# Kernel tuning notes

Hardware: AMD Instinct MI355X
Metric: run time of the kernel (lower is better)

## Reference

```python
import jax, jax.numpy as jnp
import numpy as np

B, T, I, H, L, C = 256, 512, 128, 256, 2, 1000


def _uniform(key, shape, k):
    return jax.random.uniform(key, shape, jnp.float32, -k, k)


def setup_inputs() -> dict:
    key = jax.random.key(0)
    ks = jax.random.split(key, 12)
    k = 1.0 / np.sqrt(H)
    return {
        "x": jax.random.normal(ks[0], (B, T, I), jnp.float32),
        # layer 0 (PyTorch LSTM param layout: W_ih [4H, in], W_hh [4H, H], biases [4H])
        "Wih0": _uniform(ks[1], (4 * H, I), k),
        "Whh0": _uniform(ks[2], (4 * H, H), k),
        "bih0": _uniform(ks[3], (4 * H,), k),
        "bhh0": _uniform(ks[4], (4 * H,), k),
        # layer 1
        "Wih1": _uniform(ks[5], (4 * H, H), k),
        "Whh1": _uniform(ks[6], (4 * H, H), k),
        "bih1": _uniform(ks[7], (4 * H,), k),
        "bhh1": _uniform(ks[8], (4 * H,), k),
        # final classifier
        "fcW": _uniform(ks[9], (C, H), k),
        "fcb": _uniform(ks[10], (C,), k),
    }


def _lstm_layer(seq, Wih, Whh, bias):
    # seq: [B, T, in]; returns hidden sequence [B, T, H]
    b, t = seq.shape[0], seq.shape[1]
    h_dim = Whh.shape[1]
    # Precompute input projection for all timesteps (one big GEMM).
    x_proj = jnp.einsum('bti,gi->btg', seq, Wih) + bias  # [B, T, 4H]

    def step(carry, xp):
        h, c = carry
        gates = xp + h @ Whh.T                     # [B, 4H]
        i, f, g, o = jnp.split(gates, 4, axis=-1)  # PyTorch gate order i,f,g,o
        i = jax.nn.sigmoid(i)
        f = jax.nn.sigmoid(f)
        g = jnp.tanh(g)
        o = jax.nn.sigmoid(o)
        c = f * c + i * g
        h = o * jnp.tanh(c)
        return (h, c), h

    h0 = jnp.zeros((b, h_dim), seq.dtype)
    c0 = jnp.zeros((b, h_dim), seq.dtype)
    _, hs = jax.lax.scan(step, (h0, c0), jnp.swapaxes(x_proj, 0, 1))  # [T, B, H]
    return jnp.swapaxes(hs, 0, 1)


def reference(x, Wih0, Whh0, bih0, bhh0, Wih1, Whh1, bih1, bhh1, fcW, fcb):
    out = _lstm_layer(x, Wih0, Whh0, bih0 + bhh0)
    out = _lstm_layer(out, Wih1, Whh1, bih1 + bhh1)
    # classifier on last timestep
    return out[:, -1, :] @ fcW.T + fcb  # [B, C]
```

## Files before the change

kernel.cpp:

```cpp
#include <hip/hip_runtime.h>

#define B_ 256
#define T_ 512
#define I_ 128
#define H_ 256
#define C_ 1000

#define RSTR 17

#define WT_OFF   393216
#define WT_FLOATS 917504
#define WS_NEED_FLOATS (WT_OFF + WT_FLOATS)

__device__ __forceinline__ float fsig(float x) { return 1.0f / (1.0f + __expf(-x)); }
__device__ __forceinline__ float ftanh(float x) { return 2.0f / (1.0f + __expf(-2.0f * x)) - 1.0f; }

__global__ __launch_bounds__(256) void transpose_w(
    const float* __restrict__ Wih0, const float* __restrict__ Whh0,
    const float* __restrict__ Wih1, const float* __restrict__ Whh1,
    float* __restrict__ ws)
{
    int idx = blockIdx.x * 256 + threadIdx.x;
    float* wt = ws + WT_OFF;
    if (idx < 131072) { int k = idx >> 10, r = idx & 1023; wt[idx] = Wih0[r * I_ + k]; return; }
    idx -= 131072; wt += 131072;
    if (idx < 262144) { int k = idx >> 10, r = idx & 1023; wt[idx] = Whh0[r * H_ + k]; return; }
    idx -= 262144; wt += 262144;
    if (idx < 262144) { int k = idx >> 10, r = idx & 1023; wt[idx] = Wih1[r * H_ + k]; return; }
    idx -= 262144; wt += 262144;
    { int k = idx >> 10, r = idx & 1023; wt[idx] = Whh1[r * H_ + k]; }
}

__global__ __launch_bounds__(256) void lstm_step_t(
    const float* __restrict__ x,
    const float* __restrict__ bih0, const float* __restrict__ bhh0,
    const float* __restrict__ bih1, const float* __restrict__ bhh1,
    float* __restrict__ ws, int s)
{
    __shared__ float As[128 * 36];
    __shared__ float Wsh[128 * 36];

    float* h0t = ws;
    float* h1t = ws + 2 * B_ * H_;
    float* c0 = ws + 4 * B_ * H_;
    float* c1 = ws + 5 * B_ * H_;

    const int w = blockIdx.x;
    const int layer = w >> 8;
    const int r = w & 255;
    const int bb = r >> 5;
    const int hb = r & 31;

    if (layer == 0 && s >= T_) return;
    if (layer == 1 && s < 1) return;
    const int t = (layer == 0) ? s : (s - 1);

    const float* hprev_t; const float* h0cur_t = nullptr;
    float* hout_t; float* cbuf;
    const float* bi; const float* bh;
    const float* wt_ih; const float* wt_hh;
    int nchunks;
    if (layer == 0) {
        hprev_t = h0t + ((t - 1) & 1) * B_ * H_;
        hout_t  = h0t + (t & 1) * B_ * H_;
        cbuf = c0; bi = bih0; bh = bhh0;
        wt_ih = ws + WT_OFF;
        wt_hh = ws + WT_OFF + 131072;
        nchunks = 3;
    } else {
        h0cur_t = h0t + (t & 1) * B_ * H_;
        hprev_t = h1t + ((t - 1) & 1) * B_ * H_;
        hout_t  = h1t + (t & 1) * B_ * H_;
        cbuf = c1; bi = bih1; bh = bhh1;
        wt_ih = ws + WT_OFF + 393216;
        wt_hh = ws + WT_OFF + 655360;
        nchunks = 4;
    }

    const int tid = threadIdx.x;
    const int srow = tid >> 3;
    const int kv = tid & 7;
    const int wave = tid >> 6;
    const int lane = tid & 63;
    const int br = lane >> 3;
    const int gc8 = lane & 7;
    const int krow = tid >> 1;
    const int half = tid & 1;

    float acc[4][4];
#pragma unroll
    for (int a = 0; a < 4; ++a)
#pragma unroll
        for (int b = 0; b < 4; ++b) acc[a][b] = 0.0f;

    for (int cc = 0; cc < nchunks; ++cc) {
        if (layer == 0 && cc == 0) {
            const float* ap = x + ((size_t)(bb * 32 + srow) * T_ + t) * I_;
#pragma unroll
            for (int i = 0; i < 4; ++i) {
                const int k4 = (kv + 8 * i) * 4;
                float4 va = *(const float4*)(ap + k4);
                As[(k4 + 0) * 36 + srow] = va.x;
                As[(k4 + 1) * 36 + srow] = va.y;
                As[(k4 + 2) * 36 + srow] = va.z;
                As[(k4 + 3) * 36 + srow] = va.w;
            }
        } else {
            const float* hsrc; int k0;
            if (layer == 0) { hsrc = hprev_t; k0 = (cc - 1) * 128; }
            else if (cc < 2) { hsrc = h0cur_t; k0 = cc * 128; }
            else             { hsrc = hprev_t; k0 = (cc - 2) * 128; }
            const float* asrc = hsrc + (size_t)(k0 + krow) * B_ + bb * 32 + half * 16;
            float4 a0 = ((const float4*)asrc)[0];
            float4 a1 = ((const float4*)asrc)[1];
            float4 a2 = ((const float4*)asrc)[2];
            float4 a3 = ((const float4*)asrc)[3];
            float* adst = As + krow * 36 + half * 16;
            ((float4*)adst)[0] = a0;
            ((float4*)adst)[1] = a1;
            ((float4*)adst)[2] = a2;
            ((float4*)adst)[3] = a3;
        }
        {
            const float* wtc; int k0w;
            if (layer == 0) {
                if (cc == 0) { wtc = wt_ih; k0w = 0; }
                else         { wtc = wt_hh; k0w = (cc - 1) * 128; }
            } else {
                if (cc < 2)  { wtc = wt_ih; k0w = cc * 128; }
                else         { wtc = wt_hh; k0w = (cc - 2) * 128; }
            }
            const float* wsrc = wtc + (size_t)(k0w + krow) * 1024 + (2 * half) * 256 + hb * 8;
            float4 w0 = ((const float4*)wsrc)[0];
            float4 w1 = ((const float4*)wsrc)[1];
            float4 w2 = ((const float4*)(wsrc + 256))[0];
            float4 w3 = ((const float4*)(wsrc + 256))[1];
            float* wdst = Wsh + krow * 36 + half * 16;
            ((float4*)wdst)[0] = w0;
            ((float4*)wdst)[1] = w1;
            ((float4*)wdst)[2] = w2;
            ((float4*)wdst)[3] = w3;
        }
        __syncthreads();
        const float* Ap = &As[(wave * 32) * 36 + br * 4];
        const float* Wp = &Wsh[(wave * 32) * 36 + gc8 * 4];
#pragma unroll
        for (int kk = 0; kk < 32; ++kk) {
            float4 a = *(const float4*)(Ap + kk * 36);
            float4 wv = *(const float4*)(Wp + kk * 36);
            acc[0][0] += a.x * wv.x; acc[0][1] += a.x * wv.y; acc[0][2] += a.x * wv.z; acc[0][3] += a.x * wv.w;
            acc[1][0] += a.y * wv.x; acc[1][1] += a.y * wv.y; acc[1][2] += a.y * wv.z; acc[1][3] += a.y * wv.w;
            acc[2][0] += a.z * wv.x; acc[2][1] += a.z * wv.y; acc[2][2] += a.z * wv.z; acc[2][3] += a.z * wv.w;
            acc[3][0] += a.w * wv.x; acc[3][1] += a.w * wv.y; acc[3][2] += a.w * wv.z; acc[3][3] += a.w * wv.w;
        }
        __syncthreads();
    }

    float* red = As;
    {
        const int base = tid * RSTR;
#pragma unroll
        for (int a = 0; a < 4; ++a)
#pragma unroll
            for (int b = 0; b < 4; ++b)
                red[base + a * 4 + b] = acc[a][b];
    }
    __syncthreads();
    {
        const int bl = tid >> 3;
        const int j = tid & 7;
        float g4[4];
#pragma unroll
        for (int g = 0; g < 4; ++g) {
            const int gc = g * 8 + j;
            const int br2 = bl >> 2, bi2 = bl & 3, gq = gc >> 2, gj = gc & 3;
            float v = 0.0f;
#pragma unroll
            for (int wv = 0; wv < 4; ++wv)
                v += red[(wv * 64 + br2 * 8 + gq) * RSTR + bi2 * 4 + gj];
            const int growg = g * H_ + hb * 8 + j;
            v += bi[growg] + bh[growg];
            g4[g] = v;
        }
        const float ig = fsig(g4[0]);
        const float fg = fsig(g4[1]);
        const float gg = ftanh(g4[2]);
        const float og = fsig(g4[3]);
        const int b = bb * 32 + bl;
        const int hidx = hb * 8 + j;
        const int ci = b * H_ + hidx;
        const float cn = fg * cbuf[ci] + ig * gg;
        cbuf[ci] = cn;
        hout_t[(size_t)hidx * B_ + b] = og * ftanh(cn);
    }
}

__global__ __launch_bounds__(256) void fc_kernel_t(
    const float* __restrict__ ws, const float* __restrict__ fcW,
    const float* __restrict__ fcb, float* __restrict__ out)
{
    __shared__ float As[128 * 36];
    __shared__ float Wsh[128 * 36];

    const float* h1 = ws + 3 * B_ * H_;
    const int bb = blockIdx.x >> 5;
    const int cb = blockIdx.x & 31;
    const int tid = threadIdx.x;
    const int srow = tid >> 3;
    const int kv = tid & 7;
    const int wave = tid >> 6;
    const int lane = tid & 63;
    const int br = lane >> 3;
    const int gc8 = lane & 7;
    const int crow = cb * 32 + srow;
    const int krow = tid >> 1;
    const int half = tid & 1;

    float acc[4][4];
#pragma unroll
    for (int a = 0; a < 4; ++a)
#pragma unroll
        for (int b = 0; b < 4; ++b) acc[a][b] = 0.0f;

    for (int cc = 0; cc < 2; ++cc) {
        {
            const float* asrc = h1 + (size_t)(cc * 128 + krow) * B_ + bb * 32 + half * 16;
            float4 a0 = ((const float4*)asrc)[0];
            float4 a1 = ((const float4*)asrc)[1];
            float4 a2 = ((const float4*)asrc)[2];
            float4 a3 = ((const float4*)asrc)[3];
            float* adst = As + krow * 36 + half * 16;
            ((float4*)adst)[0] = a0;
            ((float4*)adst)[1] = a1;
            ((float4*)adst)[2] = a2;
            ((float4*)adst)[3] = a3;
        }
#pragma unroll
        for (int i = 0; i < 4; ++i) {
            const int k4 = (kv + 8 * i) * 4;
            float4 vw = make_float4(0.f, 0.f, 0.f, 0.f);
            if (crow < C_) vw = *(const float4*)(fcW + crow * H_ + cc * 128 + k4);
            Wsh[(k4 + 0) * 36 + srow] = vw.x;
            Wsh[(k4 + 1) * 36 + srow] = vw.y;
            Wsh[(k4 + 2) * 36 + srow] = vw.z;
            Wsh[(k4 + 3) * 36 + srow] = vw.w;
        }
        __syncthreads();
        const float* Ap = &As[(wave * 32) * 36 + br * 4];
        const float* Wp = &Wsh[(wave * 32) * 36 + gc8 * 4];
#pragma unroll
        for (int kk = 0; kk < 32; ++kk) {
            float4 a = *(const float4*)(Ap + kk * 36);
            float4 wv = *(const float4*)(Wp + kk * 36);
            acc[0][0] += a.x * wv.x; acc[0][1] += a.x * wv.y; acc[0][2] += a.x * wv.z; acc[0][3] += a.x * wv.w;
            acc[1][0] += a.y * wv.x; acc[1][1] += a.y * wv.y; acc[1][2] += a.y * wv.z; acc[1][3] += a.y * wv.w;
            acc[2][0] += a.z * wv.x; acc[2][1] += a.z * wv.y; acc[2][2] += a.z * wv.z; acc[2][3] += a.z * wv.w;
            acc[3][0] += a.w * wv.x; acc[3][1] += a.w * wv.y; acc[3][2] += a.w * wv.z; acc[3][3] += a.w * wv.w;
        }
        __syncthreads();
    }

    float* red = As;
    {
        const int base = tid * RSTR;
#pragma unroll
        for (int a = 0; a < 4; ++a)
#pragma unroll
            for (int b = 0; b < 4; ++b)
                red[base + a * 4 + b] = acc[a][b];
    }
    __syncthreads();
    {
        const int bl = tid >> 3;
        const int j = tid & 7;
#pragma unroll
        for (int g = 0; g < 4; ++g) {
            const int gc = g * 8 + j;
            const int br2 = bl >> 2, bi2 = bl & 3, gq = gc >> 2, gj = gc & 3;
            float v = 0.0f;
#pragma unroll
            for (int wv = 0; wv < 4; ++wv)
                v += red[(wv * 64 + br2 * 8 + gq) * RSTR + bi2 * 4 + gj];
            const int cglob = cb * 32 + gc;
            if (cglob < C_) {
                v += fcb[cglob];
                out[(size_t)(bb * 32 + bl) * C_ + cglob] = v;
            }
        }
    }
}

__global__ __launch_bounds__(256) void lstm_step(
    const float* __restrict__ x,
    const float* __restrict__ Wih0, const float* __restrict__ Whh0,
    const float* __restrict__ bih0, const float* __restrict__ bhh0,
    const float* __restrict__ Wih1, const float* __restrict__ Whh1,
    const float* __restrict__ bih1, const float* __restrict__ bhh1,
    float* __restrict__ ws, int s)
{
    __shared__ float As[128 * 36];
    __shared__ float Wsh[128 * 36];

    float* h0buf = ws;
    float* h1buf = ws + 2 * B_ * H_;
    float* c0 = ws + 4 * B_ * H_;
    float* c1 = ws + 5 * B_ * H_;

    const int w = blockIdx.x;
    const int layer = w >> 8;
    const int r = w & 255;
    const int bb = r >> 5;
    const int hb = r & 31;

    if (layer == 0 && s >= T_) return;
    if (layer == 1 && s < 1) return;
    const int t = (layer == 0) ? s : (s - 1);

    const float* hprev; const float* h0cur = nullptr;
    float* hout; float* cbuf;
    const float* Wih; const float* Whh; const float* bi; const float* bh;
    int nchunks;
    if (layer == 0) {
        hprev = h0buf + ((t - 1) & 1) * B_ * H_;
        hout  = h0buf + (t & 1) * B_ * H_;
        cbuf = c0; Wih = Wih0; Whh = Whh0; bi = bih0; bh = bhh0;
        nchunks = 3;
    } else {
        h0cur = h0buf + (t & 1) * B_ * H_;
        hprev = h1buf + ((t - 1) & 1) * B_ * H_;
        hout  = h1buf + (t & 1) * B_ * H_;
        cbuf = c1; Wih = Wih1; Whh = Whh1; bi = bih1; bh = bhh1;
        nchunks = 4;
    }

    const int tid = threadIdx.x;
    const int srow = tid >> 3;
    const int kv = tid & 7;
    const int wave = tid >> 6;
    const int lane = tid & 63;
    const int br = lane >> 3;
    const int gc8 = lane & 7;
    const int grow = (srow >> 3) * H_ + hb * 8 + (srow & 7);

    float acc[4][4];
#pragma unroll
    for (int a = 0; a < 4; ++a)
#pragma unroll
        for (int b = 0; b < 4; ++b) acc[a][b] = 0.0f;

    for (int cc = 0; cc < nchunks; ++cc) {
        const float* ap;
        const float* wp;
        if (layer == 0) {
            if (cc == 0) { ap = x + ((size_t)(bb * 32 + srow) * T_ + t) * I_; wp = Wih + grow * I_; }
            else         { ap = hprev + (bb * 32 + srow) * H_ + (cc - 1) * 128; wp = Whh + grow * H_ + (cc - 1) * 128; }
        } else {
            if (cc < 2)  { ap = h0cur + (bb * 32 + srow) * H_ + cc * 128;       wp = Wih + grow * H_ + cc * 128; }
            else         { ap = hprev + (bb * 32 + srow) * H_ + (cc - 2) * 128; wp = Whh + grow * H_ + (cc - 2) * 128; }
        }
#pragma unroll
        for (int i = 0; i < 4; ++i) {
            const int k4 = (kv + 8 * i) * 4;
            float4 va = *(const float4*)(ap + k4);
            As[(k4 + 0) * 36 + srow] = va.x;
            As[(k4 + 1) * 36 + srow] = va.y;
            As[(k4 + 2) * 36 + srow] = va.z;
            As[(k4 + 3) * 36 + srow] = va.w;
            float4 vw = *(const float4*)(wp + k4);
            Wsh[(k4 + 0) * 36 + srow] = vw.x;
            Wsh[(k4 + 1) * 36 + srow] = vw.y;
            Wsh[(k4 + 2) * 36 + srow] = vw.z;
            Wsh[(k4 + 3) * 36 + srow] = vw.w;
        }
        __syncthreads();
        const float* Ap = &As[(wave * 32) * 36 + br * 4];
        const float* Wp = &Wsh[(wave * 32) * 36 + gc8 * 4];
#pragma unroll
        for (int kk = 0; kk < 32; ++kk) {
            float4 a = *(const float4*)(Ap + kk * 36);
            float4 wv = *(const float4*)(Wp + kk * 36);
            acc[0][0] += a.x * wv.x; acc[0][1] += a.x * wv.y; acc[0][2] += a.x * wv.z; acc[0][3] += a.x * wv.w;
            acc[1][0] += a.y * wv.x; acc[1][1] += a.y * wv.y; acc[1][2] += a.y * wv.z; acc[1][3] += a.y * wv.w;
            acc[2][0] += a.z * wv.x; acc[2][1] += a.z * wv.y; acc[2][2] += a.z * wv.z; acc[2][3] += a.z * wv.w;
            acc[3][0] += a.w * wv.x; acc[3][1] += a.w * wv.y; acc[3][2] += a.w * wv.z; acc[3][3] += a.w * wv.w;
        }
        __syncthreads();
    }

    float* red = As;
    {
        const int base = tid * RSTR;
#pragma unroll
        for (int a = 0; a < 4; ++a)
#pragma unroll
            for (int b = 0; b < 4; ++b)
                red[base + a * 4 + b] = acc[a][b];
    }
    __syncthreads();
    {
        const int bl = tid >> 3;
        const int j = tid & 7;
        float g4[4];
#pragma unroll
        for (int g = 0; g < 4; ++g) {
            const int gc = g * 8 + j;
            const int br2 = bl >> 2, bi2 = bl & 3, gq = gc >> 2, gj = gc & 3;
            float v = 0.0f;
#pragma unroll
            for (int wv = 0; wv < 4; ++wv)
                v += red[(wv * 64 + br2 * 8 + gq) * RSTR + bi2 * 4 + gj];
            const int growg = g * H_ + hb * 8 + j;
            v += bi[growg] + bh[growg];
            g4[g] = v;
        }
        const float ig = fsig(g4[0]);
        const float fg = fsig(g4[1]);
        const float gg = ftanh(g4[2]);
        const float og = fsig(g4[3]);
        const int b = bb * 32 + bl;
        const int hidx = hb * 8 + j;
        const int ci = b * H_ + hidx;
        const float cn = fg * cbuf[ci] + ig * gg;
        cbuf[ci] = cn;
        hout[ci] = og * ftanh(cn);
    }
}

__global__ __launch_bounds__(256) void fc_kernel(
    const float* __restrict__ ws, const float* __restrict__ fcW,
    const float* __restrict__ fcb, float* __restrict__ out)
{
    __shared__ float As[128 * 36];
    __shared__ float Wsh[128 * 36];

    const float* h1 = ws + 3 * B_ * H_;
    const int bb = blockIdx.x >> 5;
    const int cb = blockIdx.x & 31;
    const int tid = threadIdx.x;
    const int srow = tid >> 3;
    const int kv = tid & 7;
    const int wave = tid >> 6;
    const int lane = tid & 63;
    const int br = lane >> 3;
    const int gc8 = lane & 7;
    const int crow = cb * 32 + srow;

    float acc[4][4];
#pragma unroll
    for (int a = 0; a < 4; ++a)
#pragma unroll
        for (int b = 0; b < 4; ++b) acc[a][b] = 0.0f;

    for (int cc = 0; cc < 2; ++cc) {
        const float* ap = h1 + (bb * 32 + srow) * H_ + cc * 128;
#pragma unroll
        for (int i = 0; i < 4; ++i) {
            const int k4 = (kv + 8 * i) * 4;
            float4 va = *(const float4*)(ap + k4);
            As[(k4 + 0) * 36 + srow] = va.x;
            As[(k4 + 1) * 36 + srow] = va.y;
            As[(k4 + 2) * 36 + srow] = va.z;
            As[(k4 + 3) * 36 + srow] = va.w;
            float4 vw = make_float4(0.f, 0.f, 0.f, 0.f);
            if (crow < C_) vw = *(const float4*)(fcW + crow * H_ + cc * 128 + k4);
            Wsh[(k4 + 0) * 36 + srow] = vw.x;
            Wsh[(k4 + 1) * 36 + srow] = vw.y;
            Wsh[(k4 + 2) * 36 + srow] = vw.z;
            Wsh[(k4 + 3) * 36 + srow] = vw.w;
        }
        __syncthreads();
        const float* Ap = &As[(wave * 32) * 36 + br * 4];
        const float* Wp = &Wsh[(wave * 32) * 36 + gc8 * 4];
#pragma unroll
        for (int kk = 0; kk < 32; ++kk) {
            float4 a = *(const float4*)(Ap + kk * 36);
            float4 wv = *(const float4*)(Wp + kk * 36);
            acc[0][0] += a.x * wv.x; acc[0][1] += a.x * wv.y; acc[0][2] += a.x * wv.z; acc[0][3] += a.x * wv.w;
            acc[1][0] += a.y * wv.x; acc[1][1] += a.y * wv.y; acc[1][2] += a.y * wv.z; acc[1][3] += a.y * wv.w;
            acc[2][0] += a.z * wv.x; acc[2][1] += a.z * wv.y; acc[2][2] += a.z * wv.z; acc[2][3] += a.z * wv.w;
            acc[3][0] += a.w * wv.x; acc[3][1] += a.w * wv.y; acc[3][2] += a.w * wv.z; acc[3][3] += a.w * wv.w;
        }
        __syncthreads();
    }

    float* red = As;
    {
        const int base = tid * RSTR;
#pragma unroll
        for (int a = 0; a < 4; ++a)
#pragma unroll
            for (int b = 0; b < 4; ++b)
                red[base + a * 4 + b] = acc[a][b];
    }
    __syncthreads();
    {
        const int bl = tid >> 3;
        const int j = tid & 7;
#pragma unroll
        for (int g = 0; g < 4; ++g) {
            const int gc = g * 8 + j;
            const int br2 = bl >> 2, bi2 = bl & 3, gq = gc >> 2, gj = gc & 3;
            float v = 0.0f;
#pragma unroll
            for (int wv = 0; wv < 4; ++wv)
                v += red[(wv * 64 + br2 * 8 + gq) * RSTR + bi2 * 4 + gj];
            const int cglob = cb * 32 + gc;
            if (cglob < C_) {
                v += fcb[cglob];
                out[(size_t)(bb * 32 + bl) * C_ + cglob] = v;
            }
        }
    }
}

extern "C" void kernel_launch(void* const* d_in, const int* in_sizes, int n_in,
                              void* d_out, int out_size, void* d_ws, size_t ws_size,
                              hipStream_t stream)
{
    const float* x    = (const float*)d_in[0];
    const float* Wih0 = (const float*)d_in[1];
    const float* Whh0 = (const float*)d_in[2];
    const float* bih0 = (const float*)d_in[3];
    const float* bhh0 = (const float*)d_in[4];
    const float* Wih1 = (const float*)d_in[5];
    const float* Whh1 = (const float*)d_in[6];
    const float* bih1 = (const float*)d_in[7];
    const float* bhh1 = (const float*)d_in[8];
    const float* fcW  = (const float*)d_in[9];
    const float* fcb  = (const float*)d_in[10];
    float* ws  = (float*)d_ws;
    float* out = (float*)d_out;

    hipMemsetAsync(d_ws, 0, (size_t)6 * B_ * H_ * sizeof(float), stream);

    const bool use_t = ws_size >= (size_t)WS_NEED_FLOATS * sizeof(float);

    if (use_t) {
        transpose_w<<<WT_FLOATS / 256, 256, 0, stream>>>(Wih0, Whh0, Wih1, Whh1, ws);
        for (int s = 0; s <= T_; ++s) {
            lstm_step_t<<<512, 256, 0, stream>>>(x, bih0, bhh0, bih1, bhh1, ws, s);
        }
        fc_kernel_t<<<256, 256, 0, stream>>>(ws, fcW, fcb, out);
    } else {
        for (int s = 0; s <= T_; ++s) {
            lstm_step<<<512, 256, 0, stream>>>(x, Wih0, Whh0, bih0, bhh0,
                                               Wih1, Whh1, bih1, bhh1, ws, s);
        }
        fc_kernel<<<256, 256, 0, stream>>>(ws, fcW, fcb, out);
    }
}
```

Measured before the change: 6.935 ms.

## Double per-block gate tile width to halve LSTM step grid

Each block of the per-timestep LSTM kernel now computes 16 hidden units (64 gate columns) instead of 8, so each thread accumulates a 4x8 register tile and the grid per step drops from 512 to 256 blocks. This halves redundant loads of the activation tile across blocks and raises arithmetic intensity per LDS read. The cost is more registers and a larger shared-memory weight buffer, with fewer blocks in flight per step on a wide GPU. The cross-wave reduction and the gate epilogue are rewritten for the wider tile.

```diff
diff --git a/kernel.cpp b/kernel.cpp
--- a/kernel.cpp
+++ b/kernel.cpp
@@ -7,6 +7,7 @@
 #define C_ 1000
 
 #define RSTR 17
+#define RSTR2 33
 
 #define WT_OFF   393216
 #define WT_FLOATS 917504
@@ -31,14 +32,14 @@
     { int k = idx >> 10, r = idx & 1023; wt[idx] = Whh1[r * H_ + k]; }
 }
 
-__global__ __launch_bounds__(256) void lstm_step_t(
+__global__ __launch_bounds__(256) void lstm_step_t2(
     const float* __restrict__ x,
     const float* __restrict__ bih0, const float* __restrict__ bhh0,
     const float* __restrict__ bih1, const float* __restrict__ bhh1,
     float* __restrict__ ws, int s)
 {
     __shared__ float As[128 * 36];
-    __shared__ float Wsh[128 * 36];
+    __shared__ float Wsh[128 * 68];
 
     float* h0t = ws;
     float* h1t = ws + 2 * B_ * H_;
@@ -46,10 +47,10 @@
     float* c1 = ws + 5 * B_ * H_;
 
     const int w = blockIdx.x;
-    const int layer = w >> 8;
-    const int r = w & 255;
-    const int bb = r >> 5;
-    const int hb = r & 31;
+    const int layer = w >> 7;
+    const int r = w & 127;
+    const int bb = r >> 4;
+    const int gb = r & 15;
 
     if (layer == 0 && s >= T_) return;
     if (layer == 1 && s < 1) return;
@@ -87,11 +88,11 @@
     const int krow = tid >> 1;
     const int half = tid & 1;
 
-    float acc[4][4];
+    float acc[4][8];
 #pragma unroll
     for (int a = 0; a < 4; ++a)
 #pragma unroll
-        for (int b = 0; b < 4; ++b) acc[a][b] = 0.0f;
+        for (int g = 0; g < 8; ++g) acc[a][g] = 0.0f;
 
     for (int cc = 0; cc < nchunks; ++cc) {
         if (layer == 0 && cc == 0) {
@@ -130,68 +131,86 @@
                 if (cc < 2)  { wtc = wt_ih; k0w = cc * 128; }
                 else         { wtc = wt_hh; k0w = (cc - 2) * 128; }
             }
-            const float* wsrc = wtc + (size_t)(k0w + krow) * 1024 + (2 * half) * 256 + hb * 8;
-            float4 w0 = ((const float4*)wsrc)[0];
-            float4 w1 = ((const float4*)wsrc)[1];
-            float4 w2 = ((const float4*)(wsrc + 256))[0];
-            float4 w3 = ((const float4*)(wsrc + 256))[1];
-            float* wdst = Wsh + krow * 36 + half * 16;
+            const float* wsrc = wtc + (size_t)(k0w + krow) * 1024 + gb * 16;
+            const float* s0 = wsrc + (2 * half) * 256;
+            const float* s1 = wsrc + (2 * half + 1) * 256;
+            float4 w0 = ((const float4*)s0)[0];
+            float4 w1 = ((const float4*)s0)[1];
+            float4 w2 = ((const float4*)s0)[2];
+            float4 w3 = ((const float4*)s0)[3];
+            float4 w4 = ((const float4*)s1)[0];
+            float4 w5 = ((const float4*)s1)[1];
+            float4 w6 = ((const float4*)s1)[2];
+            float4 w7 = ((const float4*)s1)[3];
+            float* wdst = Wsh + krow * 68 + half * 32;
             ((float4*)wdst)[0] = w0;
             ((float4*)wdst)[1] = w1;
             ((float4*)wdst)[2] = w2;
             ((float4*)wdst)[3] = w3;
+            ((float4*)(wdst + 16))[0] = w4;
+            ((float4*)(wdst + 16))[1] = w5;
+            ((float4*)(wdst + 16))[2] = w6;
+            ((float4*)(wdst + 16))[3] = w7;
         }
         __syncthreads();
         const float* Ap = &As[(wave * 32) * 36 + br * 4];
-        const float* Wp = &Wsh[(wave * 32) * 36 + gc8 * 4];
+        const float* Wp = &Wsh[(wave * 32) * 68 + gc8 * 8];
 #pragma unroll
         for (int kk = 0; kk < 32; ++kk) {
-            float4 a = *(const float4*)(Ap + kk * 36);
-            float4 wv = *(const float4*)(Wp + kk * 36);
-            acc[0][0] += a.x * wv.x; acc[0][1] += a.x * wv.y; acc[0][2] += a.x * wv.z; acc[0][3] += a.x * wv.w;
-            acc[1][0] += a.y * wv.x; acc[1][1] += a.y * wv.y; acc[1][2] += a.y * wv.z; acc[1][3] += a.y * wv.w;
-            acc[2][0] += a.z * wv.x; acc[2][1] += a.z * wv.y; acc[2][2] += a.z * wv.z; acc[2][3] += a.z * wv.w;
-            acc[3][0] += a.w * wv.x; acc[3][1] += a.w * wv.y; acc[3][2] += a.w * wv.z; acc[3][3] += a.w * wv.w;
-        }
-        __syncthreads();
-    }
-
-    float* red = As;
-    {
-        const int base = tid * RSTR;
+            float4 a  = *(const float4*)(Ap + kk * 36);
+            float4 w0 = *(const float4*)(Wp + kk * 68);
+            float4 w1 = *(const float4*)(Wp + kk * 68 + 4);
+            acc[0][0] += a.x * w0.x; acc[0][1] += a.x * w0.y; acc[0][2] += a.x * w0.z; acc[0][3] += a.x * w0.w;
+            acc[0][4] += a.x * w1.x; acc[0][5] += a.x * w1.y; acc[0][6] += a.x * w1.z; acc[0][7] += a.x * w1.w;
+            acc[1][0] += a.y * w0.x; acc[1][1] += a.y * w0.y; acc[1][2] += a.y * w0.z; acc[1][3] += a.y * w0.w;
+            acc[1][4] += a.y * w1.x; acc[1][5] += a.y * w1.y; acc[1][6] += a.y * w1.z; acc[1][7] += a.y * w1.w;
+            acc[2][0] += a.z * w0.x; acc[2][1] += a.z * w0.y; acc[2][2] += a.z * w0.z; acc[2][3] += a.z * w0.w;
+            acc[2][4] += a.z * w1.x; acc[2][5] += a.z * w1.y; acc[2][6] += a.z * w1.z; acc[2][7] += a.z * w1.w;
+            acc[3][0] += a.w * w0.x; acc[3][1] += a.w * w0.y; acc[3][2] += a.w * w0.z; acc[3][3] += a.w * w0.w;
+            acc[3][4] += a.w * w1.x; acc[3][5] += a.w * w1.y; acc[3][6] += a.w * w1.z; acc[3][7] += a.w * w1.w;
+        }
+        __syncthreads();
+    }
+
+    float* red = Wsh;
+    {
+        const int base = (wave * 64 + lane) * RSTR2;
 #pragma unroll
         for (int a = 0; a < 4; ++a)
 #pragma unroll
-            for (int b = 0; b < 4; ++b)
-                red[base + a * 4 + b] = acc[a][b];
+            for (int g = 0; g < 8; ++g)
+                red[base + a * 8 + g] = acc[a][g];
     }
     __syncthreads();
     {
         const int bl = tid >> 3;
-        const int j = tid & 7;
-        float g4[4];
-#pragma unroll
-        for (int g = 0; g < 4; ++g) {
-            const int gc = g * 8 + j;
-            const int br2 = bl >> 2, bi2 = bl & 3, gq = gc >> 2, gj = gc & 3;
-            float v = 0.0f;
-#pragma unroll
-            for (int wv = 0; wv < 4; ++wv)
-                v += red[(wv * 64 + br2 * 8 + gq) * RSTR + bi2 * 4 + gj];
-            const int growg = g * H_ + hb * 8 + j;
-            v += bi[growg] + bh[growg];
-            g4[g] = v;
-        }
-        const float ig = fsig(g4[0]);
-        const float fg = fsig(g4[1]);
-        const float gg = ftanh(g4[2]);
-        const float og = fsig(g4[3]);
-        const int b = bb * 32 + bl;
-        const int hidx = hb * 8 + j;
-        const int ci = b * H_ + hidx;
-        const float cn = fg * cbuf[ci] + ig * gg;
-        cbuf[ci] = cn;
-        hout_t[(size_t)hidx * B_ + b] = og * ftanh(cn);
+        const int j2 = tid & 7;
+#pragma unroll
+        for (int u = 0; u < 2; ++u) {
+            const int hl = j2 * 2 + u;
+            float g4[4];
+#pragma unroll
+            for (int g = 0; g < 4; ++g) {
+                const int rr = g * 16 + hl;
+                float v = 0.0f;
+#pragma unroll
+                for (int wv = 0; wv < 4; ++wv)
+                    v += red[(wv * 64 + (bl >> 2) * 8 + (rr >> 3)) * RSTR2 + (bl & 3) * 8 + (rr & 7)];
+                const int hidx = gb * 16 + hl;
+                v += bi[g * H_ + hidx] + bh[g * H_ + hidx];
+                g4[g] = v;
+            }
+            const float ig = fsig(g4[0]);
+            const float fg = fsig(g4[1]);
+            const float gg = ftanh(g4[2]);
+            const float og = fsig(g4[3]);
+            const int b = bb * 32 + bl;
+            const int hidx = gb * 16 + hl;
+            const int ci = b * H_ + hidx;
+            const float cn = fg * cbuf[ci] + ig * gg;
+            cbuf[ci] = cn;
+            hout_t[(size_t)hidx * B_ + b] = og * ftanh(cn);
+        }
     }
 }
 
@@ -538,7 +557,7 @@
     if (use_t) {
         transpose_w<<<WT_FLOATS / 256, 256, 0, stream>>>(Wih0, Whh0, Wih1, Whh1, ws);
         for (int s = 0; s <= T_; ++s) {
-            lstm_step_t<<<512, 256, 0, stream>>>(x, bih0, bhh0, bih1, bhh1, ws, s);
+            lstm_step_t2<<<256, 256, 0, stream>>>(x, bih0, bhh0, bih1, bhh1, ws, s);
         }
         fc_kernel_t<<<256, 256, 0, stream>>>(ws, fcW, fcb, out);
     } else {
```

After: 8.552 ms. 1.23x slower.
